# Kernel tuning notes

Hardware: AMD Instinct MI355X
Metric: run time of the kernel (lower is better)

## Reference

```python
import jax, jax.numpy as jnp
import numpy as np

B, T, D = 128, 256, 1024   # batch, input_steps, input_dim
H, V, S = 1024, 1024, 128  # hidden_dim, output_dim, output_seq_length


def setup_inputs() -> dict:
    key = jax.random.key(0)
    ks = jax.random.split(key, 16)
    def w(k, shape, fan_in):
        bound = 1.0 / np.sqrt(fan_in)
        return jax.random.uniform(k, shape, jnp.float32, -bound, bound)
    return {
        "h": jax.random.normal(ks[0], (B, T, D), jnp.float32),
        # linear_h_a: Linear(D, H, bias=False); torch weight is (out, in)
        "w_h_a": w(ks[1], (H, D), D),
        # linear_s_a: Linear(H, H, bias=True)
        "w_s_a": w(ks[2], (H, H), H),
        "b_s_a": w(ks[3], (H,), H),
        # linear_a: Linear(H, 1, bias=False)
        "w_a": w(ks[4], (1, H), H),
        # linear_init_s: Linear(D, H, bias=True)
        "w_init_s": w(ks[5], (H, D), D),
        "b_init_s": w(ks[6], (H,), D),
        # GRUCell(V + D, H)
        "gru_w_ih": w(ks[7], (3 * H, V + D), H),
        "gru_w_hh": w(ks[8], (3 * H, H), H),
        "gru_b_ih": w(ks[9], (3 * H,), H),
        "gru_b_hh": w(ks[10], (3 * H,), H),
        # RNNCell(H + D, V), tanh nonlinearity
        "rnn_w_ih": w(ks[11], (V, H + D), V),
        "rnn_w_hh": w(ks[12], (V, V), V),
        "rnn_b_ih": w(ks[13], (V,), V),
        "rnn_b_hh": w(ks[14], (V,), V),
    }


def reference(h, w_h_a, w_s_a, b_s_a, w_a, w_init_s, b_init_s,
              gru_w_ih, gru_w_hh, gru_b_ih, gru_b_hh,
              rnn_w_ih, rnn_w_hh, rnn_b_ih, rnn_b_hh):
    wh = jnp.einsum('btd,hd->bth', h, w_h_a)                 # precomputed W_h @ h
    s0 = jnp.tanh(h[:, 0, :] @ w_init_s.T + b_init_s)        # (B, H)
    y0 = jnp.zeros((h.shape[0], rnn_w_ih.shape[0]), h.dtype)  # (B, V)

    def step(carry, _):
        s, y = carry
        # additive (Bahdanau) attention scores over input steps
        e = jnp.tanh(wh + (s @ w_s_a.T + b_s_a)[:, None, :])  # (B, T, H)
        scores = jnp.einsum('bth,h->bt', e, w_a[0])           # (B, T)
        a = jax.nn.softmax(scores, axis=1)
        c = jnp.einsum('bt,btd->bd', a, h)                    # context (B, D)
        # GRUCell: input = [c, y_prev], hidden = s
        x = jnp.concatenate([c, y], axis=1)
        gi = x @ gru_w_ih.T + gru_b_ih
        gh = s @ gru_w_hh.T + gru_b_hh
        ir, iz, inn = jnp.split(gi, 3, axis=1)
        hr, hz, hn = jnp.split(gh, 3, axis=1)
        r = jax.nn.sigmoid(ir + hr)
        z = jax.nn.sigmoid(iz + hz)
        n = jnp.tanh(inn + r * hn)
        s_new = (1.0 - z) * n + z * s
        # RNNCell(tanh): input = [c, s_new], hidden = y_prev; then softmax
        xr = jnp.concatenate([c, s_new], axis=1)
        pre = xr @ rnn_w_ih.T + rnn_b_ih + y @ rnn_w_hh.T + rnn_b_hh
        y_new = jax.nn.softmax(jnp.tanh(pre), axis=1)
        return (s_new, y_new), y_new

    _, ys = jax.lax.scan(step, (s0, y0), None, length=S)      # ys: (S, B, V)
    return jnp.transpose(ys, (1, 0, 2))                       # (B, S, V)
```

## Files before the change

### kernel.cpp

```cpp
#include <hip/hip_runtime.h>

typedef __bf16 bf16;
typedef __bf16 v8bf __attribute__((ext_vector_type(8)));
typedef __bf16 v4bf __attribute__((ext_vector_type(4)));
typedef float  v4f  __attribute__((ext_vector_type(4)));


static __device__ __forceinline__ float fast_tanh(float x) {
  x = fminf(fmaxf(x, -10.f), 10.f);
  float e = __expf(2.f * x);
  return (e - 1.f) * __builtin_amdgcn_rcpf(e + 1.f);
}
static __device__ __forceinline__ float fast_sigmoid(float x) {
  return __builtin_amdgcn_rcpf(1.f + __expf(-x));
}

static __device__ __forceinline__ size_t packOffN(int r, int k, int nksb) {
  return ((size_t)((r >> 4) * nksb + (k >> 5)) * 64 + ((k >> 3) & 3) * 16 + (r & 15)) * 8 + (k & 7);
}

template<int NKS, int NKSB>
static __device__ __forceinline__ void gemmTile(const bf16* __restrict__ Ap,
                                                const bf16* __restrict__ Bp,
                                                int m0, int n0, int ks0,
                                                v4f acc[2][2]) {
  const int lane = threadIdx.x & 63;
  const int w = threadIdx.x >> 6;
  const int wr = w >> 1, wc = w & 1;
  const bf16* a0p = Ap + (((size_t)((m0 >> 4) + wr * 2) * NKSB + ks0) * 64 + lane) * 8;
  const bf16* b0p = Bp + (((size_t)((n0 >> 4) + wc * 2) * NKSB + ks0) * 64 + lane) * 8;
#pragma unroll 8
  for (int ks = 0; ks < NKS; ks++) {
    v8bf a0 = *(const v8bf*)(a0p);
    v8bf a1 = *(const v8bf*)(a0p + NKSB * 512);
    v8bf b0 = *(const v8bf*)(b0p);
    v8bf b1 = *(const v8bf*)(b0p + NKSB * 512);
    a0p += 512; b0p += 512;
    acc[0][0] = __builtin_amdgcn_mfma_f32_16x16x32_bf16(a0, b0, acc[0][0], 0, 0, 0);
    acc[0][1] = __builtin_amdgcn_mfma_f32_16x16x32_bf16(a0, b1, acc[0][1], 0, 0, 0);
    acc[1][0] = __builtin_amdgcn_mfma_f32_16x16x32_bf16(a1, b0, acc[1][0], 0, 0, 0);
    acc[1][1] = __builtin_amdgcn_mfma_f32_16x16x32_bf16(a1, b1, acc[1][1], 0, 0, 0);
  }
}

static __device__ __forceinline__ void storeTileF32(float* __restrict__ C, int ldc,
                                                    int m0, int n0, v4f acc[2][2]) {
  const int lane = threadIdx.x & 63, w = threadIdx.x >> 6;
  const int wr = w >> 1, wc = w & 1;
  const int mB = m0 + wr * 32 + (lane >> 4) * 4;
  const int nB = n0 + wc * 32 + (lane & 15);
#pragma unroll
  for (int mf = 0; mf < 2; mf++)
#pragma unroll
    for (int nf = 0; nf < 2; nf++)
#pragma unroll
      for (int i = 0; i < 4; i++)
        C[(size_t)(mB + mf * 16 + i) * ldc + nB + nf * 16] = acc[mf][nf][i];
}

__global__ __launch_bounds__(256) void kPackG(const float* __restrict__ src, int ld,
                                              bf16* __restrict__ dst, int nTh, int r0) {
  int th = blockIdx.x * 256 + threadIdx.x;
  if (th >= nTh) return;
  int rb = th >> 11, ks = (th >> 6) & 31, l = th & 63;
  int r = rb * 16 + (l & 15);
  int k = ks * 32 + ((l >> 4) & 3) * 8;
  const float* s = src + (size_t)r * ld + k;
  v4f v0 = *(const v4f*)(s);
  v4f v1 = *(const v4f*)(s + 4);
  v8bf o;
#pragma unroll
  for (int e = 0; e < 4; e++) { o[e] = (bf16)v0[e]; o[4 + e] = (bf16)v1[e]; }
  *(v8bf*)(dst + packOffN(r0 + r, k, 32)) = o;
}

__global__ __launch_bounds__(256) void kPackW(const float* __restrict__ gih,
                                              const float* __restrict__ rih,
                                              const float* __restrict__ rhh,
                                              bf16* __restrict__ dst) {
  const int th = blockIdx.x * 256 + threadIdx.x;
  const int rb = th >> 12;
  const int ks = (th >> 6) & 63;
  const int l = th & 63;
  const int n = rb * 16 + (l & 15);
  const int k = ks * 32 + ((l >> 4) & 3) * 8;
  const int g = (n >> 4) & 3;
  const int j = ((n >> 6) << 4) | (n & 15);
  const float* s;
  if (g < 3)            s = gih + (size_t)(g * 1024 + j) * 2048 + k;
  else if (k < 1024)    s = rih + (size_t)j * 2048 + k;
  else                  s = rhh + (size_t)j * 1024 + (k - 1024);
  v4f v0 = *(const v4f*)(s);
  v4f v1 = *(const v4f*)(s + 4);
  v8bf o;
#pragma unroll
  for (int e = 0; e < 4; e++) { o[e] = (bf16)v0[e]; o[4 + e] = (bf16)v1[e]; }
  *(v8bf*)(dst + (size_t)th * 8) = o;
}

__global__ __launch_bounds__(256) void kCast4(const float* __restrict__ src,
                                              bf16* __restrict__ dst, int n4) {
  int i = blockIdx.x * 256 + threadIdx.x;
  if (i < n4) {
    v4f v = ((const v4f*)src)[i];
    ((v4bf*)dst)[i] = __builtin_convertvector(v, v4bf);
  }
}

__global__ __launch_bounds__(256) void kPrep(const float* __restrict__ rnn_b_ih,
                                             const float* __restrict__ rnn_b_hh,
                                             const float* __restrict__ w_a,
                                             float* __restrict__ bsum,
                                             float* __restrict__ wsum,
                                             bf16* __restrict__ xcatp) {
  __shared__ float sred[4];
  if (blockIdx.x < 64) {
    int th = blockIdx.x * 256 + threadIdx.x;
    int rb = th >> 11, ks = 64 + ((th >> 6) & 31), l = th & 63;
    v8bf z = {};
    *(v8bf*)(xcatp + ((size_t)(rb * 96 + ks) * 64 + l) * 8) = z;
  } else {
    int t = threadIdx.x;
    v4f a = *(const v4f*)(rnn_b_ih + t * 4);
    v4f c = *(const v4f*)(rnn_b_hh + t * 4);
    *(v4f*)(bsum + t * 4) = a + c;
    float zz = w_a[t] + w_a[256 + t] + w_a[512 + t] + w_a[768 + t];
#pragma unroll
    for (int off = 32; off; off >>= 1) zz += __shfl_down(zz, off, 64);
    if ((t & 63) == 0) sred[t >> 6] = zz;
    __syncthreads();
    if (t == 0) wsum[0] = sred[0] + sred[1] + sred[2] + sred[3];
  }
}

__global__ __launch_bounds__(256) void kGemmE(const bf16* __restrict__ Ap,
                                              const bf16* __restrict__ Bp,
                                              bf16* __restrict__ C) {
  const int nt = blockIdx.x & 15, mt = blockIdx.x >> 4;
  v4f acc[2][2] = {};
  gemmTile<32, 32>(Ap, Bp, mt * 64, nt * 64, 0, acc);
  const int lane = threadIdx.x & 63, w = threadIdx.x >> 6;
  const int wr = w >> 1, wc = w & 1;
  const int mB = mt * 64 + wr * 32 + (lane >> 4) * 4;
  const int nB = nt * 64 + wc * 32 + (lane & 15);
#pragma unroll
  for (int mf = 0; mf < 2; mf++)
#pragma unroll
    for (int nf = 0; nf < 2; nf++)
#pragma unroll
      for (int i = 0; i < 4; i++)
        C[(size_t)(mB + mf * 16 + i) * 1024 + nB + nf * 16] = (bf16)__expf(2.f * acc[mf][nf][i]);
}

__global__ __launch_bounds__(256) void kGemmS0(const bf16* __restrict__ Ap,
                                               const bf16* __restrict__ Bp,
                                               const float* __restrict__ bias,
                                               float* __restrict__ sF, bf16* __restrict__ sB) {
  const int nt = blockIdx.x & 15, mt = blockIdx.x >> 4;
  v4f acc[2][2] = {};
  gemmTile<32, 32>(Ap, Bp, mt * 64, nt * 64, 0, acc);
  const int lane = threadIdx.x & 63, w = threadIdx.x >> 6;
  const int wr = w >> 1, wc = w & 1;
  const int mB = mt * 64 + wr * 32 + (lane >> 4) * 4;
  const int nB = nt * 64 + wc * 32 + (lane & 15);
#pragma unroll
  for (int mf = 0; mf < 2; mf++)
#pragma unroll
    for (int nf = 0; nf < 2; nf++) {
      const int n = nB + nf * 16;
      float bv = bias[n];
#pragma unroll
      for (int i = 0; i < 4; i++) {
        const int m = mB + mf * 16 + i;
        float v = fast_tanh(acc[mf][nf][i] + bv);
        size_t pi = packOffN(m, n, 32);
        sF[pi] = v;
        sB[pi] = (bf16)v;
      }
    }
}

__global__ __launch_bounds__(256) void kGemmPS(const bf16* __restrict__ Ap,
                                               const bf16* __restrict__ Bp,
                                               float* __restrict__ PS0, float* __restrict__ PS1) {
  const int t = blockIdx.x;
  const int kh = t & 1, mh = (t >> 1) & 1, nt = t >> 2;
  v4f acc[2][2] = {};
  gemmTile<16, 32>(Ap, Bp, mh * 64, nt * 64, kh * 16, acc);
  storeTileF32(kh ? PS1 : PS0, 5120, mh * 64, nt * 64, acc);
}


static __device__ __forceinline__ void outPhase256(
    int b, int step,
    const float* __restrict__ PS0, const float* __restrict__ PS1,
    const float* __restrict__ gcpR, const float* __restrict__ bsum,
    float* __restrict__ out, bf16* __restrict__ xcatp, float* smred) {
  const int tid = threadIdx.x, lane = tid & 63, w = tid >> 6;
  const int v0 = tid * 4;
  const size_t o5 = (size_t)b * 5120 + v0;
  const size_t oR = (size_t)b * 1024 + v0;
  v4f pre = *(const v4f*)(PS0 + o5);
  pre += *(const v4f*)(PS1 + o5);
  pre += *(const v4f*)(gcpR + oR);
  pre += *(const v4f*)(bsum + v0);
  float ee[4]; float psum = 0.f;
#pragma unroll
  for (int i = 0; i < 4; i++) { ee[i] = __expf(fast_tanh(pre[i])); psum += ee[i]; }
#pragma unroll
  for (int off = 32; off; off >>= 1) psum += __shfl_down(psum, off, 64);
  if (lane == 0) smred[w] = psum;
  __syncthreads();
  const float rden = __builtin_amdgcn_rcpf(smred[0] + smred[1] + smred[2] + smred[3]);
  v4f y4;
#pragma unroll
  for (int i = 0; i < 4; i++) y4[i] = ee[i] * rden;
  *(v4f*)(out + ((size_t)b * 128 + step) * 1024 + v0) = y4;
  v4bf yb;
#pragma unroll
  for (int i = 0; i < 4; i++) yb[i] = (bf16)y4[i];
  *(v4bf*)(xcatp + packOffN(b, 2048 + v0, 96)) = yb;
}

__global__ __launch_bounds__(256) void kFused1(
    const float* __restrict__ PS0, const float* __restrict__ PS1,
    const float* __restrict__ b_s_a, const float* __restrict__ w_a,
    const float* __restrict__ wsum,
    const bf16* __restrict__ Eb, const bf16* __restrict__ hb,
    const float* __restrict__ gcpR, const float* __restrict__ bsum,
    float* __restrict__ Zpart, float* __restrict__ out,
    bf16* __restrict__ xcatp, int step) {
  __shared__ float sF[1024];
  __shared__ float sP[128];
  __shared__ float sred[4];
  const int tid = threadIdx.x, lane = tid & 63, w = tid >> 6;
  if (blockIdx.x >= 256) {
    if (step == 0) return;
    outPhase256(blockIdx.x - 256, step - 1, PS0, PS1, gcpR, bsum, out, xcatp, sred);
    return;
  }
  const int b = blockIdx.x >> 1, half = blockIdx.x & 1;
  {
    const int i = tid * 4;
    const size_t o = (size_t)b * 5120 + 1024 + i;
    v4f sa0 = *(const v4f*)(PS0 + o);
    v4f sa1 = *(const v4f*)(PS1 + o);
    v4f bsa = *(const v4f*)(b_s_a + i);
    v4f f;
#pragma unroll
    for (int e = 0; e < 4; e++) f[e] = __expf(2.f * (sa0[e] + sa1[e] + bsa[e]));
    *(v4f*)&sF[i] = f;
  }
  __syncthreads();
  float Fr[16], wv[16];
  const int h0 = lane * 16;
#pragma unroll
  for (int jj = 0; jj < 4; jj++) {
    *(v4f*)&Fr[jj * 4] = *(const v4f*)&sF[h0 + jj * 4];
    *(v4f*)&wv[jj * 4] = *(const v4f*)(w_a + h0 + jj * 4);
  }
  const float Wsum = wsum[0];
  const bf16* Erow = Eb + ((size_t)b * 256 + half * 128 + w * 32) * 1024 + h0;
  for (int ti = 0; ti < 32; ti++) {
    v8bf ea = *(const v8bf*)(Erow);
    v8bf eb2 = *(const v8bf*)(Erow + 8);
    Erow += 1024;
    float acc = 0.f;
#pragma unroll
    for (int jp = 0; jp < 4; jp++) {
      float d0 = __builtin_fmaf((float)ea[2 * jp],     Fr[2 * jp],     1.f);
      float d1 = __builtin_fmaf((float)ea[2 * jp + 1], Fr[2 * jp + 1], 1.f);
      float nu = wv[2 * jp] * d1;
      nu = __builtin_fmaf(wv[2 * jp + 1], d0, nu);
      acc = __builtin_fmaf(nu, __builtin_amdgcn_rcpf(d0 * d1), acc);
      float t0 = __builtin_fmaf((float)eb2[2 * jp],     Fr[8 + 2 * jp],     1.f);
      float t1 = __builtin_fmaf((float)eb2[2 * jp + 1], Fr[8 + 2 * jp + 1], 1.f);
      float nu2 = wv[8 + 2 * jp] * t1;
      nu2 = __builtin_fmaf(wv[8 + 2 * jp + 1], t0, nu2);
      acc = __builtin_fmaf(nu2, __builtin_amdgcn_rcpf(t0 * t1), acc);
    }
#pragma unroll
    for (int off = 32; off; off >>= 1) acc += __shfl_down(acc, off, 64);
    if (lane == 0) sP[w * 32 + ti] = __expf(Wsum - 2.f * acc);
  }
  __syncthreads();
  float zv = (tid < 128) ? sP[tid] : 0.f;
#pragma unroll
  for (int off = 32; off; off >>= 1) zv += __shfl_down(zv, off, 64);
  if (lane == 0) sred[w] = zv;
  __syncthreads();
  if (tid == 0) Zpart[2 * b + half] = sred[0] + sred[1] + sred[2] + sred[3];
  const int d0 = tid * 4;
  const bf16* hp = hb + (size_t)b * 262144 + (size_t)half * 131072 + d0;
  v4f cacc = {};
#pragma unroll 8
  for (int t = 0; t < 128; t++) {
    v4bf h4 = *(const v4bf*)hp;
    hp += 1024;
    cacc += sP[t] * __builtin_convertvector(h4, v4f);
  }
  v4bf cb;
#pragma unroll
  for (int e = 0; e < 4; e++) cb[e] = (bf16)cacc[e];
  *(v4bf*)(xcatp + packOffN(b, half * 1024 + d0, 96)) = cb;
}

__global__ __launch_bounds__(768) void kXGru(
    const bf16* __restrict__ xcatp, const bf16* __restrict__ Wbigp,
    const float* __restrict__ PS0, const float* __restrict__ PS1,
    const float* __restrict__ gru_b_ih, const float* __restrict__ gru_b_hh,
    const float* __restrict__ Zpart,
    float* __restrict__ s_f32p, bf16* __restrict__ s_b16p,
    float* __restrict__ gcpR) {
  __shared__ float tl[3][64][68];
  const int tid = threadIdx.x, lane = tid & 63, w = tid >> 6;
  const int mh = blockIdx.x & 1, Jb = blockIdx.x >> 1;
  const int kg = w >> 2, q = w & 3;
  const int rb0 = mh * 4 + (q >> 1) * 2;
  const int nb0 = Jb * 4 + (q & 1) * 2;
  const int ksA = kg * 32;
  const int ksB = (kg == 2) ? 32 : 0;
  v4f acc[2][2] = {};
  const bf16* a0p = xcatp + (((size_t)rb0 * 96 + ksA) * 64 + lane) * 8;
  const bf16* b0p = Wbigp + (((size_t)nb0 * 64 + ksB) * 64 + lane) * 8;
#pragma unroll 8
  for (int ks = 0; ks < 32; ks++) {
    v8bf a0 = *(const v8bf*)(a0p);
    v8bf a1 = *(const v8bf*)(a0p + 96 * 512);
    v8bf b0 = *(const v8bf*)(b0p);
    v8bf b1 = *(const v8bf*)(b0p + 64 * 512);
    a0p += 512; b0p += 512;
    acc[0][0] = __builtin_amdgcn_mfma_f32_16x16x32_bf16(a0, b0, acc[0][0], 0, 0, 0);
    acc[0][1] = __builtin_amdgcn_mfma_f32_16x16x32_bf16(a0, b1, acc[0][1], 0, 0, 0);
    acc[1][0] = __builtin_amdgcn_mfma_f32_16x16x32_bf16(a1, b0, acc[1][0], 0, 0, 0);
    acc[1][1] = __builtin_amdgcn_mfma_f32_16x16x32_bf16(a1, b1, acc[1][1], 0, 0, 0);
  }
  const int lr = (q >> 1) * 32 + ((lane >> 4) << 2);
  const int lc = (q & 1) * 32 + (lane & 15);
#pragma unroll
  for (int af = 0; af < 2; af++)
#pragma unroll
    for (int bq = 0; bq < 2; bq++)
#pragma unroll
      for (int i = 0; i < 4; i++)
        tl[kg][lr + af * 16 + i][lc + bq * 16] = acc[af][bq][i];
  __syncthreads();
  if (tid >= 512) return;
  const int r = tid >> 3;
  const int jo = (tid & 7) * 2;
  const int row = mh * 64 + r;
  const int jbase = Jb * 16 + jo;
  const float rden = __builtin_amdgcn_rcpf(Zpart[2 * row] + Zpart[2 * row + 1]);
  const size_t pb = (size_t)row * 5120;
#pragma unroll
  for (int u = 0; u < 2; u++) {
    const int jj = jbase + u;
    const int cc = jo + u;
    float ir_ = (tl[0][r][cc]      + tl[1][r][cc])      * rden + tl[2][r][cc]      + gru_b_ih[jj];
    float iz_ = (tl[0][r][16 + cc] + tl[1][r][16 + cc]) * rden + tl[2][r][16 + cc] + gru_b_ih[1024 + jj];
    float in_ = (tl[0][r][32 + cc] + tl[1][r][32 + cc]) * rden + tl[2][r][32 + cc] + gru_b_ih[2048 + jj];
    float pr_ = (tl[0][r][48 + cc] + tl[1][r][48 + cc]) * rden + tl[2][r][48 + cc];
    float hr = PS0[pb + 2048 + jj] + PS1[pb + 2048 + jj] + gru_b_hh[jj];
    float hz = PS0[pb + 3072 + jj] + PS1[pb + 3072 + jj] + gru_b_hh[1024 + jj];
    float hn = PS0[pb + 4096 + jj] + PS1[pb + 4096 + jj] + gru_b_hh[2048 + jj];
    float rg = fast_sigmoid(ir_ + hr);
    float zg = fast_sigmoid(iz_ + hz);
    float ng = fast_tanh(in_ + rg * hn);
    size_t sp = packOffN(row, jj, 32);
    float sv = s_f32p[sp];
    float sn = (1.f - zg) * ng + zg * sv;
    s_f32p[sp] = sn;
    s_b16p[sp] = (bf16)sn;
    gcpR[(size_t)row * 1024 + jj] = pr_;
  }
}

__global__ __launch_bounds__(256) void kOutFinal(
    const float* __restrict__ PS0, const float* __restrict__ PS1,
    const float* __restrict__ gcpR, const float* __restrict__ bsum,
    float* __restrict__ out, bf16* __restrict__ xcatp) {
  __shared__ float smred[4];
  outPhase256(blockIdx.x, 127, PS0, PS1, gcpR, bsum, out, xcatp, smred);
}

extern "C" void kernel_launch(void* const* d_in, const int* in_sizes, int n_in,
                              void* d_out, int out_size, void* d_ws, size_t ws_size,
                              hipStream_t stream) {
  const float* h        = (const float*)d_in[0];
  const float* w_h_a    = (const float*)d_in[1];
  const float* w_s_a    = (const float*)d_in[2];
  const float* b_s_a    = (const float*)d_in[3];
  const float* w_a      = (const float*)d_in[4];
  const float* w_init_s = (const float*)d_in[5];
  const float* b_init_s = (const float*)d_in[6];
  const float* gru_w_ih = (const float*)d_in[7];
  const float* gru_w_hh = (const float*)d_in[8];
  const float* gru_b_ih = (const float*)d_in[9];
  const float* gru_b_hh = (const float*)d_in[10];
  const float* rnn_w_ih = (const float*)d_in[11];
  const float* rnn_w_hh = (const float*)d_in[12];
  const float* rnn_b_ih = (const float*)d_in[13];
  const float* rnn_b_hh = (const float*)d_in[14];
  (void)in_sizes; (void)n_in; (void)out_size; (void)ws_size;

  char* p = (char*)d_ws;
  auto alloc = [&](size_t bytes) { char* r = p; p += (bytes + 255) & ~(size_t)255; return r; };
  bf16* hbig   = (bf16*)alloc(33554432ull * 2);
  bf16* Eb     = (bf16*)alloc(33554432ull * 2);
  bf16* h0p    = (bf16*)alloc(131072ull * 2);
  bf16* wbha_p = (bf16*)alloc(1048576ull * 2);
  bf16* wbini_p= (bf16*)alloc(1048576ull * 2);
  bf16* Wbigp  = (bf16*)alloc(8388608ull * 2);
  bf16* WP5p   = (bf16*)alloc(5242880ull * 2);
  bf16* xcatp  = (bf16*)alloc(393216ull * 2);
  float* PS0   = (float*)alloc(128ull * 5120 * 4);
  float* PS1   = (float*)alloc(128ull * 5120 * 4);
  float* gcpR  = (float*)alloc(128ull * 1024 * 4);
  float* s_f32p= (float*)alloc(131072ull * 4);
  bf16* s_b16p = (bf16*)alloc(131072ull * 2);
  float* Zpart = (float*)alloc(256ull * 4);
  float* bsum  = (float*)alloc(1024ull * 4);
  float* wsum  = (float*)alloc(256);
  float* out = (float*)d_out;

  kPackG<<<dim3(16384), 256, 0, stream>>>(h, 1024, hbig, 4194304, 0);
  kPackG<<<dim3(64),    256, 0, stream>>>(h, 262144, h0p, 16384, 0);
  kPackG<<<dim3(512),   256, 0, stream>>>(w_h_a, 1024, wbha_p, 131072, 0);
  kPackG<<<dim3(512),   256, 0, stream>>>(w_init_s, 1024, wbini_p, 131072, 0);
  kPackW<<<dim3(4096),  256, 0, stream>>>(gru_w_ih, rnn_w_ih, rnn_w_hh, Wbigp);
  kPackG<<<dim3(512),   256, 0, stream>>>(rnn_w_ih + 1024, 2048, WP5p, 131072, 0);
  kPackG<<<dim3(512),   256, 0, stream>>>(w_s_a, 1024, WP5p, 131072, 1024);
  kPackG<<<dim3(1536),  256, 0, stream>>>(gru_w_hh, 1024, WP5p, 393216, 2048);
  kPrep<<<dim3(65), 256, 0, stream>>>(rnn_b_ih, rnn_b_hh, w_a, bsum, wsum, xcatp);

  kGemmE<<<dim3(8192), 256, 0, stream>>>(hbig, wbha_p, Eb);
  kCast4<<<dim3(32768), 256, 0, stream>>>(h, hbig, 8388608);
  kGemmS0<<<dim3(32), 256, 0, stream>>>(h0p, wbini_p, b_init_s, s_f32p, s_b16p);
  kGemmPS<<<dim3(320), 256, 0, stream>>>(s_b16p, WP5p, PS0, PS1);

  for (int step = 0; step < 128; step++) {
    kFused1<<<dim3(384), 256, 0, stream>>>(PS0, PS1, b_s_a, w_a, wsum, Eb, hbig,
                                           gcpR, bsum, Zpart, out, xcatp, step);
    kXGru<<<dim3(128), 768, 0, stream>>>(xcatp, Wbigp, PS0, PS1,
                                         gru_b_ih, gru_b_hh, Zpart,
                                         s_f32p, s_b16p, gcpR);
    kGemmPS<<<dim3(320), 256, 0, stream>>>(s_b16p, WP5p, PS0, PS1);
  }
  kOutFinal<<<dim3(128), 256, 0, stream>>>(PS0, PS1, gcpR, bsum, out, xcatp);
}
```

Before: 7.960 ms.

## Drop split-K in per-step GEMMs and merge K-groups within waves

```diff
diff --git a/kernel.cpp b/kernel.cpp
--- a/kernel.cpp
+++ b/kernel.cpp
@@ -180,29 +180,24 @@
     }
 }
 
-__global__ __launch_bounds__(256) void kGemmPS(const bf16* __restrict__ Ap,
-                                               const bf16* __restrict__ Bp,
-                                               float* __restrict__ PS0, float* __restrict__ PS1) {
-  const int t = blockIdx.x;
-  const int kh = t & 1, mh = (t >> 1) & 1, nt = t >> 2;
+__global__ __launch_bounds__(256) void kGemmPS1(const bf16* __restrict__ Ap,
+                                                const bf16* __restrict__ Bp,
+                                                float* __restrict__ PS) {
+  const int mh = blockIdx.x & 1, nt = blockIdx.x >> 1;
   v4f acc[2][2] = {};
-  gemmTile<16, 32>(Ap, Bp, mh * 64, nt * 64, kh * 16, acc);
-  storeTileF32(kh ? PS1 : PS0, 5120, mh * 64, nt * 64, acc);
-}
-
+  gemmTile<32, 32>(Ap, Bp, mh * 64, nt * 64, 0, acc);
+  storeTileF32(PS, 5120, mh * 64, nt * 64, acc);
+}
 
 static __device__ __forceinline__ void outPhase256(
-    int b, int step,
-    const float* __restrict__ PS0, const float* __restrict__ PS1,
+    int b, int step, const float* __restrict__ PS,
     const float* __restrict__ gcpR, const float* __restrict__ bsum,
     float* __restrict__ out, bf16* __restrict__ xcatp, float* smred) {
   const int tid = threadIdx.x, lane = tid & 63, w = tid >> 6;
   const int v0 = tid * 4;
   const size_t o5 = (size_t)b * 5120 + v0;
-  const size_t oR = (size_t)b * 1024 + v0;
-  v4f pre = *(const v4f*)(PS0 + o5);
-  pre += *(const v4f*)(PS1 + o5);
-  pre += *(const v4f*)(gcpR + oR);
+  v4f pre = *(const v4f*)(PS + o5);
+  pre += *(const v4f*)(gcpR + (size_t)b * 1024 + v0);
   pre += *(const v4f*)(bsum + v0);
   float ee[4]; float psum = 0.f;
 #pragma unroll
@@ -223,32 +218,31 @@
 }
 
 __global__ __launch_bounds__(256) void kFused1(
-    const float* __restrict__ PS0, const float* __restrict__ PS1,
-    const float* __restrict__ b_s_a, const float* __restrict__ w_a,
-    const float* __restrict__ wsum,
+    const float* __restrict__ PS, const float* __restrict__ b_s_a,
+    const float* __restrict__ w_a, const float* __restrict__ wsum,
     const bf16* __restrict__ Eb, const bf16* __restrict__ hb,
     const float* __restrict__ gcpR, const float* __restrict__ bsum,
     float* __restrict__ Zpart, float* __restrict__ out,
     bf16* __restrict__ xcatp, int step) {
-  __shared__ float sF[1024];
-  __shared__ float sP[128];
-  __shared__ float sred[4];
+  __shared__ float sm[1160];
   const int tid = threadIdx.x, lane = tid & 63, w = tid >> 6;
   if (blockIdx.x >= 256) {
     if (step == 0) return;
-    outPhase256(blockIdx.x - 256, step - 1, PS0, PS1, gcpR, bsum, out, xcatp, sred);
+    outPhase256(blockIdx.x - 256, step - 1, PS, gcpR, bsum, out, xcatp, sm + 1156);
     return;
   }
+  float* sF = sm;
+  float* sP = sm + 1024;
+  float* sred = sm + 1152;
   const int b = blockIdx.x >> 1, half = blockIdx.x & 1;
   {
     const int i = tid * 4;
     const size_t o = (size_t)b * 5120 + 1024 + i;
-    v4f sa0 = *(const v4f*)(PS0 + o);
-    v4f sa1 = *(const v4f*)(PS1 + o);
+    v4f sa = *(const v4f*)(PS + o);
     v4f bsa = *(const v4f*)(b_s_a + i);
     v4f f;
 #pragma unroll
-    for (int e = 0; e < 4; e++) f[e] = __expf(2.f * (sa0[e] + sa1[e] + bsa[e]));
+    for (int e = 0; e < 4; e++) f[e] = __expf(2.f * (sa[e] + bsa[e]));
     *(v4f*)&sF[i] = f;
   }
   __syncthreads();
@@ -305,82 +299,98 @@
   *(v4bf*)(xcatp + packOffN(b, half * 1024 + d0, 96)) = cb;
 }
 
-__global__ __launch_bounds__(768) void kXGru(
+__global__ __launch_bounds__(256) void kXGru(
     const bf16* __restrict__ xcatp, const bf16* __restrict__ Wbigp,
-    const float* __restrict__ PS0, const float* __restrict__ PS1,
-    const float* __restrict__ gru_b_ih, const float* __restrict__ gru_b_hh,
-    const float* __restrict__ Zpart,
+    const float* __restrict__ PS, const float* __restrict__ gbih,
+    const float* __restrict__ gbhh, const float* __restrict__ Zpart,
     float* __restrict__ s_f32p, bf16* __restrict__ s_b16p,
     float* __restrict__ gcpR) {
-  __shared__ float tl[3][64][68];
+  __shared__ float tl[64 * 68];
   const int tid = threadIdx.x, lane = tid & 63, w = tid >> 6;
   const int mh = blockIdx.x & 1, Jb = blockIdx.x >> 1;
-  const int kg = w >> 2, q = w & 3;
-  const int rb0 = mh * 4 + (q >> 1) * 2;
-  const int nb0 = Jb * 4 + (q & 1) * 2;
-  const int ksA = kg * 32;
-  const int ksB = (kg == 2) ? 32 : 0;
-  v4f acc[2][2] = {};
-  const bf16* a0p = xcatp + (((size_t)rb0 * 96 + ksA) * 64 + lane) * 8;
-  const bf16* b0p = Wbigp + (((size_t)nb0 * 64 + ksB) * 64 + lane) * 8;
-#pragma unroll 8
+  const int qr = w >> 1, qc = w & 1;
+  const int rb0 = mh * 4 + qr * 2;
+  const int nb0 = Jb * 4 + qc * 2;
+  v4f accC[2][2] = {};
+  v4f accY[2][2] = {};
+  const bf16* aB = xcatp + (((size_t)rb0 * 96) * 64 + lane) * 8;
+  const bf16* bB = Wbigp + (((size_t)nb0 * 64) * 64 + lane) * 8;
+#pragma unroll 2
   for (int ks = 0; ks < 32; ks++) {
-    v8bf a0 = *(const v8bf*)(a0p);
-    v8bf a1 = *(const v8bf*)(a0p + 96 * 512);
-    v8bf b0 = *(const v8bf*)(b0p);
-    v8bf b1 = *(const v8bf*)(b0p + 64 * 512);
-    a0p += 512; b0p += 512;
-    acc[0][0] = __builtin_amdgcn_mfma_f32_16x16x32_bf16(a0, b0, acc[0][0], 0, 0, 0);
-    acc[0][1] = __builtin_amdgcn_mfma_f32_16x16x32_bf16(a0, b1, acc[0][1], 0, 0, 0);
-    acc[1][0] = __builtin_amdgcn_mfma_f32_16x16x32_bf16(a1, b0, acc[1][0], 0, 0, 0);
-    acc[1][1] = __builtin_amdgcn_mfma_f32_16x16x32_bf16(a1, b1, acc[1][1], 0, 0, 0);
-  }
-  const int lr = (q >> 1) * 32 + ((lane >> 4) << 2);
-  const int lc = (q & 1) * 32 + (lane & 15);
-#pragma unroll
-  for (int af = 0; af < 2; af++)
-#pragma unroll
-    for (int bq = 0; bq < 2; bq++)
-#pragma unroll
-      for (int i = 0; i < 4; i++)
-        tl[kg][lr + af * 16 + i][lc + bq * 16] = acc[af][bq][i];
+    const bf16* a = aB + ks * 512;
+    const bf16* b = bB + ks * 512;
+    v8bf ac00 = *(const v8bf*)(a);
+    v8bf ac01 = *(const v8bf*)(a + 96 * 512);
+    v8bf ac10 = *(const v8bf*)(a + 32 * 512);
+    v8bf ac11 = *(const v8bf*)(a + 128 * 512);
+    v8bf ay0  = *(const v8bf*)(a + 64 * 512);
+    v8bf ay1  = *(const v8bf*)(a + 160 * 512);
+    v8bf bc0 = *(const v8bf*)(b);
+    v8bf bc1 = *(const v8bf*)(b + 64 * 512);
+    v8bf by0 = *(const v8bf*)(b + 32 * 512);
+    v8bf by1 = *(const v8bf*)(b + 96 * 512);
+    accC[0][0] = __builtin_amdgcn_mfma_f32_16x16x32_bf16(ac00, bc0, accC[0][0], 0, 0, 0);
+    accC[0][0] = __builtin_amdgcn_mfma_f32_16x16x32_bf16(ac10, bc0, accC[0][0], 0, 0, 0);
+    accC[0][1] = __builtin_amdgcn_mfma_f32_16x16x32_bf16(ac00, bc1, accC[0][1], 0, 0, 0);
+    accC[0][1] = __builtin_amdgcn_mfma_f32_16x16x32_bf16(ac10, bc1, accC[0][1], 0, 0, 0);
+    accC[1][0] = __builtin_amdgcn_mfma_f32_16x16x32_bf16(ac01, bc0, accC[1][0], 0, 0, 0);
+    accC[1][0] = __builtin_amdgcn_mfma_f32_16x16x32_bf16(ac11, bc0, accC[1][0], 0, 0, 0);
+    accC[1][1] = __builtin_amdgcn_mfma_f32_16x16x32_bf16(ac01, bc1, accC[1][1], 0, 0, 0);
+    accC[1][1] = __builtin_amdgcn_mfma_f32_16x16x32_bf16(ac11, bc1, accC[1][1], 0, 0, 0);
+    accY[0][0] = __builtin_amdgcn_mfma_f32_16x16x32_bf16(ay0, by0, accY[0][0], 0, 0, 0);
+    accY[0][1] = __builtin_amdgcn_mfma_f32_16x16x32_bf16(ay0, by1, accY[0][1], 0, 0, 0);
+    accY[1][0] = __builtin_amdgcn_mfma_f32_16x16x32_bf16(ay1, by0, accY[1][0], 0, 0, 0);
+    accY[1][1] = __builtin_amdgcn_mfma_f32_16x16x32_bf16(ay1, by1, accY[1][1], 0, 0, 0);
+  }
+  const int r0 = qr * 32 + ((lane >> 4) << 2);
+  const int c0 = qc * 32 + (lane & 15);
+#pragma unroll
+  for (int rf = 0; rf < 2; rf++) {
+    const int rl = r0 + rf * 16;
+    const int grow = mh * 64 + rl;
+#pragma unroll
+    for (int i = 0; i < 4; i++) {
+      const float rden = __builtin_amdgcn_rcpf(Zpart[2 * (grow + i)] + Zpart[2 * (grow + i) + 1]);
+#pragma unroll
+      for (int cf = 0; cf < 2; cf++)
+        tl[(rl + i) * 68 + c0 + cf * 16] = accC[rf][cf][i] * rden + accY[rf][cf][i];
+    }
+  }
   __syncthreads();
-  if (tid >= 512) return;
-  const int r = tid >> 3;
-  const int jo = (tid & 7) * 2;
-  const int row = mh * 64 + r;
-  const int jbase = Jb * 16 + jo;
-  const float rden = __builtin_amdgcn_rcpf(Zpart[2 * row] + Zpart[2 * row + 1]);
-  const size_t pb = (size_t)row * 5120;
-#pragma unroll
-  for (int u = 0; u < 2; u++) {
-    const int jj = jbase + u;
-    const int cc = jo + u;
-    float ir_ = (tl[0][r][cc]      + tl[1][r][cc])      * rden + tl[2][r][cc]      + gru_b_ih[jj];
-    float iz_ = (tl[0][r][16 + cc] + tl[1][r][16 + cc]) * rden + tl[2][r][16 + cc] + gru_b_ih[1024 + jj];
-    float in_ = (tl[0][r][32 + cc] + tl[1][r][32 + cc]) * rden + tl[2][r][32 + cc] + gru_b_ih[2048 + jj];
-    float pr_ = (tl[0][r][48 + cc] + tl[1][r][48 + cc]) * rden + tl[2][r][48 + cc];
-    float hr = PS0[pb + 2048 + jj] + PS1[pb + 2048 + jj] + gru_b_hh[jj];
-    float hz = PS0[pb + 3072 + jj] + PS1[pb + 3072 + jj] + gru_b_hh[1024 + jj];
-    float hn = PS0[pb + 4096 + jj] + PS1[pb + 4096 + jj] + gru_b_hh[2048 + jj];
-    float rg = fast_sigmoid(ir_ + hr);
-    float zg = fast_sigmoid(iz_ + hz);
-    float ng = fast_tanh(in_ + rg * hn);
-    size_t sp = packOffN(row, jj, 32);
-    float sv = s_f32p[sp];
-    float sn = (1.f - zg) * ng + zg * sv;
-    s_f32p[sp] = sn;
-    s_b16p[sp] = (bf16)sn;
-    gcpR[(size_t)row * 1024 + jj] = pr_;
-  }
+  const int r = tid >> 2, jb0 = (tid & 3) * 4;
+  const int grow = mh * 64 + r;
+  const int j0 = Jb * 16 + jb0;
+  const float* tr = tl + r * 68;
+  v4f ir4 = *(const v4f*)(tr + jb0)      + *(const v4f*)(gbih + j0);
+  v4f iz4 = *(const v4f*)(tr + 16 + jb0) + *(const v4f*)(gbih + 1024 + j0);
+  v4f in4 = *(const v4f*)(tr + 32 + jb0) + *(const v4f*)(gbih + 2048 + j0);
+  v4f pr4 = *(const v4f*)(tr + 48 + jb0);
+  const size_t pb = (size_t)grow * 5120;
+  v4f hr4 = *(const v4f*)(PS + pb + 2048 + j0) + *(const v4f*)(gbhh + j0);
+  v4f hz4 = *(const v4f*)(PS + pb + 3072 + j0) + *(const v4f*)(gbhh + 1024 + j0);
+  v4f hn4 = *(const v4f*)(PS + pb + 4096 + j0) + *(const v4f*)(gbhh + 2048 + j0);
+  const size_t sp = packOffN(grow, j0, 32);
+  v4f sv = *(const v4f*)(s_f32p + sp);
+  v4f sn; v4bf snb;
+#pragma unroll
+  for (int u = 0; u < 4; u++) {
+    float rg = fast_sigmoid(ir4[u] + hr4[u]);
+    float zg = fast_sigmoid(iz4[u] + hz4[u]);
+    float ng = fast_tanh(in4[u] + rg * hn4[u]);
+    float s1 = (1.f - zg) * ng + zg * sv[u];
+    sn[u] = s1; snb[u] = (bf16)s1;
+  }
+  *(v4f*)(s_f32p + sp) = sn;
+  *(v4bf*)(s_b16p + sp) = snb;
+  *(v4f*)(gcpR + (size_t)grow * 1024 + j0) = pr4;
 }
 
 __global__ __launch_bounds__(256) void kOutFinal(
-    const float* __restrict__ PS0, const float* __restrict__ PS1,
-    const float* __restrict__ gcpR, const float* __restrict__ bsum,
-    float* __restrict__ out, bf16* __restrict__ xcatp) {
+    const float* __restrict__ PS, const float* __restrict__ gcpR,
+    const float* __restrict__ bsum, float* __restrict__ out,
+    bf16* __restrict__ xcatp) {
   __shared__ float smred[4];
-  outPhase256(blockIdx.x, 127, PS0, PS1, gcpR, bsum, out, xcatp, smred);
+  outPhase256(blockIdx.x, 127, PS, gcpR, bsum, out, xcatp, smred);
 }
 
 extern "C" void kernel_launch(void* const* d_in, const int* in_sizes, int n_in,
@@ -413,8 +423,7 @@
   bf16* Wbigp  = (bf16*)alloc(8388608ull * 2);
   bf16* WP5p   = (bf16*)alloc(5242880ull * 2);
   bf16* xcatp  = (bf16*)alloc(393216ull * 2);
-  float* PS0   = (float*)alloc(128ull * 5120 * 4);
-  float* PS1   = (float*)alloc(128ull * 5120 * 4);
+  float* PS    = (float*)alloc(128ull * 5120 * 4);
   float* gcpR  = (float*)alloc(128ull * 1024 * 4);
   float* s_f32p= (float*)alloc(131072ull * 4);
   bf16* s_b16p = (bf16*)alloc(131072ull * 2);
@@ -436,15 +445,14 @@
   kGemmE<<<dim3(8192), 256, 0, stream>>>(hbig, wbha_p, Eb);
   kCast4<<<dim3(32768), 256, 0, stream>>>(h, hbig, 8388608);
   kGemmS0<<<dim3(32), 256, 0, stream>>>(h0p, wbini_p, b_init_s, s_f32p, s_b16p);
-  kGemmPS<<<dim3(320), 256, 0, stream>>>(s_b16p, WP5p, PS0, PS1);
+  kGemmPS1<<<dim3(160), 256, 0, stream>>>(s_b16p, WP5p, PS);
 
   for (int step = 0; step < 128; step++) {
-    kFused1<<<dim3(384), 256, 0, stream>>>(PS0, PS1, b_s_a, w_a, wsum, Eb, hbig,
+    kFused1<<<dim3(384), 256, 0, stream>>>(PS, b_s_a, w_a, wsum, Eb, hbig,
                                            gcpR, bsum, Zpart, out, xcatp, step);
-    kXGru<<<dim3(128), 768, 0, stream>>>(xcatp, Wbigp, PS0, PS1,
-                                         gru_b_ih, gru_b_hh, Zpart,
-                                         s_f32p, s_b16p, gcpR);
-    kGemmPS<<<dim3(320), 256, 0, stream>>>(s_b16p, WP5p, PS0, PS1);
-  }
-  kOutFinal<<<dim3(128), 256, 0, stream>>>(PS0, PS1, gcpR, bsum, out, xcatp);
-}
+    kXGru<<<dim3(128), 256, 0, stream>>>(xcatp, Wbigp, PS, gru_b_ih, gru_b_hh,
+                                         Zpart, s_f32p, s_b16p, gcpR);
+    kGemmPS1<<<dim3(160), 256, 0, stream>>>(s_b16p, WP5p, PS);
+  }
+  kOutFinal<<<dim3(128), 256, 0, stream>>>(PS, gcpR, bsum, out, xcatp);
+}
```

Measured after the change: 10.93 ms. +37.3%, slower.
